# Optimization experiments

Measured on AMD Instinct MI355X. Metric: run time of the kernel, lower is better.

The kernel has to match this reference:

```python
import jax, jax.numpy as jnp
import numpy as np

B, H, W = 8, 160, 160
L = H * W  # 25600, matches nn.LayerNorm(25600)
QDIM = KDIM = MID = OUT = 256
HEADS = 8
HEAD_DIM = MID // HEADS  # 32
LN_EPS = 1e-5


def conv1x1(x, w, b):
    # x: [N,C,H,W], w: [O,C], b: [O] -> [N,O,H,W]
    return jnp.einsum('nchw,oc->nohw', x, w) + b[None, :, None, None]


def setup_inputs() -> dict:
    key = jax.random.key(0)
    ks = jax.random.split(key, 12)
    s = 0.02
    return {
        'query': jax.random.normal(ks[0], (B, QDIM, H, W), jnp.float32),
        'key': jax.random.normal(ks[1], (B, KDIM, H, W), jnp.float32),
        'Wq': jax.random.normal(ks[2], (MID, QDIM), jnp.float32) * s,
        'bq': jnp.zeros((MID,), jnp.float32),
        'Wk': jax.random.normal(ks[3], (MID, KDIM), jnp.float32) * s,
        'bk': jnp.zeros((MID,), jnp.float32),
        'Wv': jax.random.normal(ks[4], (MID, KDIM), jnp.float32) * s,
        'bv': jnp.zeros((MID,), jnp.float32),
        'Wo': jax.random.normal(ks[5], (OUT, MID), jnp.float32) * s,
        'bo': jnp.zeros((OUT,), jnp.float32),
        'gamma': jnp.ones((L,), jnp.float32),
        'beta': jnp.zeros((L,), jnp.float32),
    }


def reference(query, key, Wq, bq, Wk, bk, Wv, bv, Wo, bo, gamma, beta):
    # 1x1-conv projections, flatten spatial dims to L
    q = conv1x1(query, Wq, bq).reshape(B, HEADS, HEAD_DIM, L)
    k = conv1x1(key, Wk, bk).reshape(B, HEADS, HEAD_DIM, L)
    v = conv1x1(key, Wv, bv).reshape(B, HEADS, HEAD_DIM, L)
    # NOTE: faithful to the source, scores contract over L (spatial), giving
    # a [B, heads, head_dim, head_dim] channel-attention matrix.
    scores = jnp.einsum('nhdl,nhel->nhde', q, k) / (KDIM ** 0.5)
    attn = jax.nn.softmax(scores, axis=-1)  # dropout is identity at eval
    out = jnp.einsum('nhde,nhel->nhdl', attn, v).reshape(B, MID, L)
    # LayerNorm over the flattened spatial axis (size 25600)
    mu = jnp.mean(out, axis=-1, keepdims=True)
    var = jnp.var(out, axis=-1, keepdims=True)
    out = (out - mu) * jax.lax.rsqrt(var + LN_EPS) * gamma + beta
    out = out.reshape(B, MID, H, W)
    return conv1x1(out, Wo, bo)
```

## Files before the change

kernel.cpp:

```cpp
#include <hip/hip_runtime.h>
#include <hip/hip_bf16.h>
#include <stdint.h>

#define LROW 25600
#define NCH 256
#define LN_EPS 1e-5f

typedef float f32x4 __attribute__((ext_vector_type(4)));
typedef __bf16 bf16x8 __attribute__((ext_vector_type(8)));
typedef __bf16 bf16x4 __attribute__((ext_vector_type(4)));

__device__ __forceinline__ void gload_lds16(const void* g, void* l) {
  __builtin_amdgcn_global_load_lds(
      (const __attribute__((address_space(1))) void*)(uintptr_t)g,
      (__attribute__((address_space(3))) void*)(uint32_t)(uintptr_t)l,
      16, 0, 0);
}

__device__ __forceinline__ bf16x8 cvt8(f32x4 a, f32x4 b) {
  bf16x8 r;
  r[0] = (__bf16)a[0]; r[1] = (__bf16)a[1]; r[2] = (__bf16)a[2]; r[3] = (__bf16)a[3];
  r[4] = (__bf16)b[0]; r[5] = (__bf16)b[1]; r[6] = (__bf16)b[2]; r[7] = (__bf16)b[3];
  return r;
}

__global__ __launch_bounds__(512, 2) void gram_k(
    const float* __restrict__ qg, const float* __restrict__ kg,
    float* __restrict__ G, float* __restrict__ Gkk,
    float* __restrict__ sq, float* __restrict__ sk) {
  __shared__ __align__(16) float lA[2][8192];
  __shared__ __align__(16) float lB[2][8192];
  const int bid = blockIdx.x;
  const int b = bid >> 5;
  const int s = bid & 31;
  const int mat = (s < 21) ? 0 : 1;
  const int idx = mat ? (s - 21) : s;
  const int parts = mat ? 11 : 21;
  const int c0 = (800 * idx) / parts;
  const int c1 = (800 * (idx + 1)) / parts;
  const int tid = threadIdx.x;
  const int w = tid >> 6, lane = tid & 63;
  const float* Ag = (mat ? kg : qg) + (size_t)b * NCH * LROW;
  const float* Bg = kg + (size_t)b * NCH * LROW;
  float* Gout = (mat ? Gkk : G) + (size_t)b * NCH * NCH;
  float* sums = (mat ? sk : sq) + b * NCH;

  const int rb = w >> 1, chh = w & 1;

  const f32x4 zero = {0.f, 0.f, 0.f, 0.f};
  f32x4 acc[2][4][4];
#pragma unroll
  for (int t = 0; t < 2; ++t)
#pragma unroll
    for (int i = 0; i < 4; ++i)
#pragma unroll
      for (int j = 0; j < 4; ++j) acc[t][i][j] = zero;

  const int cu = (lane & 7) ^ (lane >> 3);

  auto stage = [&](int c, int d) {
#pragma unroll
    for (int i = 0; i < 4; ++i) {
      const int row = (w * 4 + i) * 8 + (lane >> 3);
      gload_lds16(Ag + (size_t)row * LROW + c * 32 + cu * 4, &lA[d][(w * 4 + i) * 256]);
    }
    if (mat == 0) {
#pragma unroll
      for (int i = 0; i < 4; ++i) {
        const int row = (w * 4 + i) * 8 + (lane >> 3);
        gload_lds16(Bg + (size_t)row * LROW + c * 32 + cu * 4, &lB[d][(w * 4 + i) * 256]);
      }
    }
  };

  float rsum = 0.f;
  const int nc = c1 - c0;
  stage(c0, 0);
  for (int cc = 0; cc < nc; ++cc) {
    const int buf = cc & 1;
    const bool pf = (cc + 1 < nc);
    if (pf) stage(c0 + cc + 1, buf ^ 1);
    if (mat == 0) {
      if (pf) asm volatile("s_waitcnt vmcnt(8)" ::: "memory");
      else    asm volatile("s_waitcnt vmcnt(0)" ::: "memory");
    } else {
      if (pf) asm volatile("s_waitcnt vmcnt(4)" ::: "memory");
      else    asm volatile("s_waitcnt vmcnt(0)" ::: "memory");
    }
    __builtin_amdgcn_s_barrier();
    __builtin_amdgcn_sched_barrier(0);

    {
      const int row = tid >> 1;
      const int ub = (tid & 1) * 4;
#pragma unroll
      for (int u = 0; u < 4; ++u) {
        f32x4 v = *(const f32x4*)&lA[buf][row * 32 + (ub + u) * 4];
        rsum += v[0] + v[1] + v[2] + v[3];
      }
    }

    bf16x8 a[4];
#pragma unroll
    for (int i = 0; i < 4; ++i) {
      const int row = rb * 64 + i * 16 + (lane & 15);
      const int u0 = (lane >> 4) * 2;
      const int s0 = u0 ^ (row & 7), s1 = (u0 + 1) ^ (row & 7);
      f32x4 f0 = *(const f32x4*)&lA[buf][row * 32 + s0 * 4];
      f32x4 f1 = *(const f32x4*)&lA[buf][row * 32 + s1 * 4];
      a[i] = cvt8(f0, f1);
    }
    const float(*lBp)[8192] = mat ? lA : lB;
#pragma unroll
    for (int t = 0; t < 2; ++t) {
#pragma unroll
      for (int j = 0; j < 4; ++j) {
        const int row = chh * 128 + t * 64 + j * 16 + (lane & 15);
        const int u0 = (lane >> 4) * 2;
        const int s0 = u0 ^ (row & 7), s1 = (u0 + 1) ^ (row & 7);
        f32x4 f0 = *(const f32x4*)&lBp[buf][row * 32 + s0 * 4];
        f32x4 f1 = *(const f32x4*)&lBp[buf][row * 32 + s1 * 4];
        bf16x8 bfrag = cvt8(f0, f1);
#pragma unroll
        for (int i = 0; i < 4; ++i)
          acc[t][i][j] = __builtin_amdgcn_mfma_f32_16x16x32_bf16(a[i], bfrag, acc[t][i][j], 0, 0, 0);
      }
    }
    asm volatile("s_waitcnt lgkmcnt(0)" ::: "memory");
    __builtin_amdgcn_s_barrier();
    __builtin_amdgcn_sched_barrier(0);
  }

  atomicAdd(&sums[tid >> 1], rsum);
#pragma unroll
  for (int t = 0; t < 2; ++t)
#pragma unroll
    for (int i = 0; i < 4; ++i)
#pragma unroll
      for (int j = 0; j < 4; ++j) {
        const int col = chh * 128 + t * 64 + j * 16 + (lane & 15);
        const int row0 = rb * 64 + i * 16 + (lane >> 4) * 4;
#pragma unroll
        for (int r = 0; r < 4; ++r)
          atomicAdd(&Gout[(row0 + r) * NCH + col], acc[t][i][j][r]);
      }
}

__global__ __launch_bounds__(256) void attn_k(
    const float* __restrict__ G, const float* __restrict__ sq,
    const float* __restrict__ sk,
    const float* __restrict__ Wq, const float* __restrict__ bq,
    const float* __restrict__ Wk, const float* __restrict__ bk,
    const float* __restrict__ Wv, const float* __restrict__ bv,
    float* __restrict__ M, float* __restrict__ cvec) {
  __shared__ float Wql[32][257];
  __shared__ float Wkl[32][257];
  __shared__ float QGl[32][257];
  __shared__ float Sl[32][33];
  __shared__ float Al[32][33];
  __shared__ float ul[32], wl[32];
  const int b = blockIdx.x >> 3, h = blockIdx.x & 7;
  const int t = threadIdx.x;
  const float* Gb = G + (size_t)b * 65536;

  for (int i = 0; i < 32; ++i) {
    int idx = i * 256 + t;
    int d = idx >> 8, c = idx & 255;
    Wql[d][c] = Wq[(h * 32 + d) * 256 + c];
    Wkl[d][c] = Wk[(h * 32 + d) * 256 + c];
  }
  __syncthreads();
  {
    float a[32];
#pragma unroll
    for (int d = 0; d < 32; ++d) a[d] = 0.f;
    for (int c = 0; c < 256; ++c) {
      float g = Gb[c * 256 + t];
#pragma unroll
      for (int d = 0; d < 32; ++d) a[d] += Wql[d][c] * g;
    }
    for (int d = 0; d < 32; ++d) QGl[d][t] = a[d];
  }
  if (t < 32) {
    float u = 0.f, wv = 0.f;
    for (int c = 0; c < 256; ++c) {
      u += Wql[t][c] * sq[b * 256 + c];
      wv += Wkl[t][c] * sk[b * 256 + c];
    }
    ul[t] = u; wl[t] = wv;
  }
  __syncthreads();
  for (int i = 0; i < 4; ++i) {
    int idx = i * 256 + t;
    int d = idx >> 5, e = idx & 31;
    float sv = 0.f;
    for (int c = 0; c < 256; ++c) sv += QGl[d][c] * Wkl[e][c];
    float bqd = bq[h * 32 + d], bke = bk[h * 32 + e];
    Sl[d][e] = (sv + ul[d] * bke + bqd * wl[e] + 25600.f * bqd * bke) * (1.f / 16.f);
  }
  __syncthreads();
  if (t < 32) {
    float m = -1e30f;
    for (int e = 0; e < 32; ++e) m = fmaxf(m, Sl[t][e]);
    float ssum = 0.f;
    for (int e = 0; e < 32; ++e) { float p = __expf(Sl[t][e] - m); Al[t][e] = p; ssum += p; }
    float is = 1.f / ssum;
    for (int e = 0; e < 32; ++e) Al[t][e] *= is;
  }
  __syncthreads();
  {
    float a[32];
#pragma unroll
    for (int d = 0; d < 32; ++d) a[d] = 0.f;
    for (int e = 0; e < 32; ++e) {
      float wv = Wv[(h * 32 + e) * 256 + t];
#pragma unroll
      for (int d = 0; d < 32; ++d) a[d] += Al[d][e] * wv;
    }
    for (int d = 0; d < 32; ++d) M[((size_t)b * 256 + h * 32 + d) * 256 + t] = a[d];
  }
  if (t < 32) {
    float cv = 0.f;
    for (int e = 0; e < 32; ++e) cv += Al[t][e] * bv[h * 32 + e];
    cvec[b * 256 + h * 32 + t] = cv;
  }
}

__global__ __launch_bounds__(256) void stats_k(
    const float* __restrict__ Gkk, const float* __restrict__ M,
    const float* __restrict__ sk, const float* __restrict__ cvec,
    float* __restrict__ mu, float* __restrict__ inv) {
  __shared__ float Ml[32][257];
  __shared__ float Ql[32][257];
  const int b = blockIdx.x >> 3, cb = blockIdx.x & 7;
  const int t = threadIdx.x;
  const float* Gk = Gkk + (size_t)b * 65536;
  for (int i = 0; i < 32; ++i) {
    int idx = i * 256 + t;
    Ml[idx >> 8][idx & 255] = M[((size_t)b * 256 + cb * 32 + (idx >> 8)) * 256 + (idx & 255)];
  }
  __syncthreads();
  {
    float a[32];
#pragma unroll
    for (int c = 0; c < 32; ++c) a[c] = 0.f;
    for (int cc = 0; cc < 256; ++cc) {
      float g = Gk[cc * 256 + t];
#pragma unroll
      for (int c = 0; c < 32; ++c) a[c] += Ml[c][cc] * g;
    }
    for (int c = 0; c < 32; ++c) Ql[c][t] = a[c];
  }
  __syncthreads();
  if (t < 32) {
    float qf = 0.f, msk = 0.f;
    for (int j = 0; j < 256; ++j) {
      qf += Ql[t][j] * Ml[t][j];
      msk += Ml[t][j] * sk[b * 256 + j];
    }
    int c = cb * 32 + t;
    float cv = cvec[b * 256 + c];
    float muv = msk * (1.f / 25600.f) + cv;
    float sum2 = qf + 2.f * cv * msk + 25600.f * cv * cv;
    float var = sum2 * (1.f / 25600.f) - muv * muv;
    mu[b * 256 + c] = muv;
    inv[b * 256 + c] = rsqrtf(var + LN_EPS);
  }
}

__global__ __launch_bounds__(256) void pmat_k(
    const float* __restrict__ M, const float* __restrict__ Wo,
    const float* __restrict__ inv, const float* __restrict__ cvec,
    const float* __restrict__ mu, __bf16* __restrict__ Pb,
    float* __restrict__ t1, float* __restrict__ wsum) {
  __shared__ float Wol[32][257];
  __shared__ float invl[256];
  const int b = blockIdx.x >> 3, ob = blockIdx.x & 7;
  const int t = threadIdx.x;
  invl[t] = inv[b * 256 + t];
  __syncthreads();
  for (int i = 0; i < 32; ++i) {
    int idx = i * 256 + t;
    int o = idx >> 8, c = idx & 255;
    Wol[o][c] = Wo[(ob * 32 + o) * 256 + c] * invl[c];
  }
  __syncthreads();
  {
    float a[32];
#pragma unroll
    for (int o = 0; o < 32; ++o) a[o] = 0.f;
    for (int c = 0; c < 256; ++c) {
      float m = M[((size_t)b * 256 + c) * 256 + t];
#pragma unroll
      for (int o = 0; o < 32; ++o) a[o] += Wol[o][c] * m;
    }
    for (int o = 0; o < 32; ++o)
      Pb[((size_t)b * 256 + ob * 32 + o) * 256 + t] = (__bf16)a[o];
  }
  if (t < 32) {
    float s1 = 0.f, s2 = 0.f;
    for (int c = 0; c < 256; ++c) {
      s1 += Wol[t][c] * (cvec[b * 256 + c] - mu[b * 256 + c]);
      s2 += Wo[(ob * 32 + t) * 256 + c];
    }
    t1[b * 256 + ob * 32 + t] = s1;
    wsum[b * 256 + ob * 32 + t] = s2;
  }
}

__global__ __launch_bounds__(512, 2) void out_k(
    const float* __restrict__ key, const __bf16* __restrict__ Pb,
    const float* __restrict__ t1, const float* __restrict__ wsum,
    const float* __restrict__ bo, const float* __restrict__ gamma,
    const float* __restrict__ beta, float* __restrict__ out) {
  __shared__ __align__(16) __bf16 Bt[256 * 256];
  const int bid = blockIdx.x;
  const int b = bid / 100, tt = bid % 100;
  const int l0 = tt * 256;
  const int tid = threadIdx.x, w = tid >> 6, lane = tid & 63;
  const float* Kb = key + (size_t)b * NCH * LROW;

  for (int i = 0; i < 32; ++i) {
    int idx = i * 512 + tid;
    int l = idx & 255, cq = idx >> 8;
    float x0 = Kb[(size_t)(cq * 4 + 0) * LROW + l0 + l];
    float x1 = Kb[(size_t)(cq * 4 + 1) * LROW + l0 + l];
    float x2 = Kb[(size_t)(cq * 4 + 2) * LROW + l0 + l];
    float x3 = Kb[(size_t)(cq * 4 + 3) * LROW + l0 + l];
    bf16x4 hv;
    hv[0] = (__bf16)x0; hv[1] = (__bf16)x1; hv[2] = (__bf16)x2; hv[3] = (__bf16)x3;
    int unit = cq >> 1;
    int byteoff = l * 512 + (((unit ^ (l & 7))) << 4) + (cq & 1) * 8;
    *(bf16x4*)((char*)Bt + byteoff) = hv;
  }
  __syncthreads();

  const int rb = w >> 1, chh = w & 1;
  const f32x4 zero = {0.f, 0.f, 0.f, 0.f};
  f32x4 acc[2][4][4];
#pragma unroll
  for (int t = 0; t < 2; ++t)
#pragma unroll
    for (int i = 0; i < 4; ++i)
#pragma unroll
      for (int j = 0; j < 4; ++j) acc[t][i][j] = zero;

#pragma unroll
  for (int ks = 0; ks < 8; ++ks) {
    bf16x8 a[4];
#pragma unroll
    for (int i = 0; i < 4; ++i) {
      const int row = rb * 64 + i * 16 + (lane & 15);
      a[i] = *(const bf16x8*)(Pb + ((size_t)b * 256 + row) * 256 + ks * 32 + (lane >> 4) * 8);
    }
#pragma unroll
    for (int t = 0; t < 2; ++t) {
#pragma unroll
      for (int j = 0; j < 4; ++j) {
        const int col = chh * 128 + t * 64 + j * 16 + (lane & 15);
        const int unit = ks * 4 + (lane >> 4);
        const int byteoff = col * 512 + ((unit ^ (col & 7)) << 4);
        bf16x8 bfrag = *(const bf16x8*)((const char*)Bt + byteoff);
#pragma unroll
        for (int i = 0; i < 4; ++i)
          acc[t][i][j] = __builtin_amdgcn_mfma_f32_16x16x32_bf16(a[i], bfrag, acc[t][i][j], 0, 0, 0);
      }
    }
  }

  float t1r[4][4], wsr[4][4], bor[4][4];
#pragma unroll
  for (int i = 0; i < 4; ++i)
#pragma unroll
    for (int r = 0; r < 4; ++r) {
      const int row = rb * 64 + i * 16 + (lane >> 4) * 4 + r;
      t1r[i][r] = t1[b * 256 + row];
      wsr[i][r] = wsum[b * 256 + row];
      bor[i][r] = bo[row];
    }
#pragma unroll
  for (int t = 0; t < 2; ++t)
#pragma unroll
    for (int j = 0; j < 4; ++j) {
      const int col = chh * 128 + t * 64 + j * 16 + (lane & 15);
      const float gm = gamma[l0 + col];
      const float bt = beta[l0 + col];
#pragma unroll
      for (int i = 0; i < 4; ++i) {
        const int row0 = rb * 64 + i * 16 + (lane >> 4) * 4;
#pragma unroll
        for (int r = 0; r < 4; ++r) {
          const int row = row0 + r;
          float v = gm * (acc[t][i][j][r] + t1r[i][r]) + bt * wsr[i][r] + bor[i][r];
          out[((size_t)b * 256 + row) * LROW + l0 + col] = v;
        }
      }
    }
}

extern "C" void kernel_launch(void* const* d_in, const int* in_sizes, int n_in,
                              void* d_out, int out_size, void* d_ws, size_t ws_size,
                              hipStream_t stream) {
  const float* query = (const float*)d_in[0];
  const float* key   = (const float*)d_in[1];
  const float* Wq = (const float*)d_in[2];
  const float* bq = (const float*)d_in[3];
  const float* Wk = (const float*)d_in[4];
  const float* bk = (const float*)d_in[5];
  const float* Wv = (const float*)d_in[6];
  const float* bv = (const float*)d_in[7];
  const float* Wo = (const float*)d_in[8];
  const float* bo = (const float*)d_in[9];
  const float* gamma = (const float*)d_in[10];
  const float* beta  = (const float*)d_in[11];
  float* out = (float*)d_out;

  float* ws = (float*)d_ws;
  float* G    = ws;
  float* Gkk  = G + 524288;
  float* sq   = Gkk + 524288;
  float* sk   = sq + 2048;
  float* M    = sk + 2048;
  float* cvec = M + 524288;
  float* mu   = cvec + 2048;
  float* inv  = mu + 2048;
  float* t1   = inv + 2048;
  float* wsum = t1 + 2048;
  __bf16* Pb  = (__bf16*)(wsum + 2048);

  hipMemsetAsync(d_ws, 0, (size_t)(524288 * 2 + 4096) * sizeof(float), stream);

  gram_k<<<256, 512, 0, stream>>>(query, key, G, Gkk, sq, sk);
  attn_k<<<64, 256, 0, stream>>>(G, sq, sk, Wq, bq, Wk, bk, Wv, bv, M, cvec);
  stats_k<<<64, 256, 0, stream>>>(Gkk, M, sk, cvec, mu, inv);
  pmat_k<<<64, 256, 0, stream>>>(M, Wo, inv, cvec, mu, Pb, t1, wsum);
  out_k<<<800, 512, 0, stream>>>(key, Pb, t1, wsum, bo, gamma, beta, out);
}
```

Before: 571.5 us.

## Cache bf16 key from gram pass, replace atomics with partials, bf16 output GEMM

The gram kernel now converts fp32 tiles to bf16 once, in registers, before writing them to LDS, using register double-buffering in place of direct global-to-LDS loads. The key-only blocks also write a bf16 copy of key to workspace. Partial Gram matrices go to per-split slices and are summed by a new reduce kernel, which removes the atomics and the large memset. The output kernel then reads the half-size bf16 key, cutting its input traffic, in exchange for extra workspace writes and an added reduce launch.

Result: slower. 673.1 us (+17.8%).

```diff
diff --git a/kernel.cpp b/kernel.cpp
--- a/kernel.cpp
+++ b/kernel.cpp
@@ -9,13 +9,7 @@
 typedef float f32x4 __attribute__((ext_vector_type(4)));
 typedef __bf16 bf16x8 __attribute__((ext_vector_type(8)));
 typedef __bf16 bf16x4 __attribute__((ext_vector_type(4)));
-
-__device__ __forceinline__ void gload_lds16(const void* g, void* l) {
-  __builtin_amdgcn_global_load_lds(
-      (const __attribute__((address_space(1))) void*)(uintptr_t)g,
-      (__attribute__((address_space(3))) void*)(uint32_t)(uintptr_t)l,
-      16, 0, 0);
-}
+typedef uint32_t u32x2 __attribute__((ext_vector_type(2)));
 
 __device__ __forceinline__ bf16x8 cvt8(f32x4 a, f32x4 b) {
   bf16x8 r;
@@ -24,126 +18,149 @@
   return r;
 }
 
-__global__ __launch_bounds__(512, 2) void gram_k(
+__device__ __forceinline__ void wg_bar() {
+  asm volatile("s_waitcnt lgkmcnt(0)\n\ts_barrier" ::: "memory");
+}
+
+template <int FULL>
+__global__ __launch_bounds__(1024, 4) void gram_k(
     const float* __restrict__ qg, const float* __restrict__ kg,
-    float* __restrict__ G, float* __restrict__ Gkk,
-    float* __restrict__ sq, float* __restrict__ sk) {
-  __shared__ __align__(16) float lA[2][8192];
-  __shared__ __align__(16) float lB[2][8192];
+    float* __restrict__ Gd, float* __restrict__ Gkkd,
+    float* __restrict__ sq, float* __restrict__ sk,
+    __bf16* __restrict__ kbf) {
+  __shared__ __align__(16) __bf16 lA[256 * 32];
+  __shared__ __align__(16) __bf16 lB[256 * 32];
   const int bid = blockIdx.x;
-  const int b = bid >> 5;
-  const int s = bid & 31;
+  const int b = bid >> 5, s = bid & 31;
   const int mat = (s < 21) ? 0 : 1;
   const int idx = mat ? (s - 21) : s;
   const int parts = mat ? 11 : 21;
-  const int c0 = (800 * idx) / parts;
-  const int c1 = (800 * (idx + 1)) / parts;
+  const int c0 = (800 * idx) / parts, c1 = (800 * (idx + 1)) / parts;
+  const int nc = c1 - c0;
   const int tid = threadIdx.x;
   const int w = tid >> 6, lane = tid & 63;
+  const int wr = w >> 2, wc = w & 3;
+  const int lr = lane & 15, g = lane >> 4;
   const float* Ag = (mat ? kg : qg) + (size_t)b * NCH * LROW;
   const float* Bg = kg + (size_t)b * NCH * LROW;
-  float* Gout = (mat ? Gkk : G) + (size_t)b * NCH * NCH;
-  float* sums = (mat ? sk : sq) + b * NCH;
-
-  const int rb = w >> 1, chh = w & 1;
+
+  const int rowS = tid >> 2, uS = tid & 3;
+  const int uSw = uS ^ ((rowS >> 1) & 3);
+  const size_t gOff = (size_t)rowS * LROW + uS * 8;
+  __bf16* ldsA_dst = lA + rowS * 32 + uSw * 8;
+  __bf16* ldsB_dst = lB + rowS * 32 + uSw * 8;
 
   const f32x4 zero = {0.f, 0.f, 0.f, 0.f};
-  f32x4 acc[2][4][4];
-#pragma unroll
-  for (int t = 0; t < 2; ++t)
+  f32x4 acc[4][4];
+#pragma unroll
+  for (int i = 0; i < 4; ++i)
+#pragma unroll
+    for (int j = 0; j < 4; ++j) acc[i][j] = zero;
+
+  float rsum = 0.f;
+
+  auto LOADG = [&](int c, f32x4* d) {
+    const float* pa = Ag + gOff + (size_t)c * 32;
+    d[0] = *(const f32x4*)pa;
+    d[1] = *(const f32x4*)(pa + 4);
+    if (mat == 0) {
+      const float* pb = Bg + gOff + (size_t)c * 32;
+      d[2] = *(const f32x4*)pb;
+      d[3] = *(const f32x4*)(pb + 4);
+    }
+  };
+
+  auto PROCESS = [&](int c, f32x4* d) {
+#pragma unroll
+    for (int e = 0; e < 4; ++e) rsum += d[0][e] + d[1][e];
+    bf16x8 av = cvt8(d[0], d[1]);
+    *(bf16x8*)ldsA_dst = av;
+    if (mat == 0) {
+      *(bf16x8*)ldsB_dst = cvt8(d[2], d[3]);
+    } else if (FULL) {
+      *(bf16x8*)(kbf + (size_t)(b * NCH + rowS) * LROW + (size_t)c * 32 + uS * 8) = av;
+    }
+    wg_bar();
+    const __bf16* Bp = mat ? lA : lB;
+    bf16x8 af[4];
+#pragma unroll
+    for (int i = 0; i < 4; ++i) {
+      const int row = wr * 64 + i * 16 + lr;
+      const int u = g ^ ((row >> 1) & 3);
+      af[i] = *(const bf16x8*)(lA + row * 32 + u * 8);
+    }
+#pragma unroll
+    for (int j = 0; j < 4; ++j) {
+      const int row = wc * 64 + j * 16 + lr;
+      const int u = g ^ ((row >> 1) & 3);
+      bf16x8 bfj = *(const bf16x8*)(Bp + row * 32 + u * 8);
+#pragma unroll
+      for (int i = 0; i < 4; ++i)
+        acc[i][j] = __builtin_amdgcn_mfma_f32_16x16x32_bf16(af[i], bfj, acc[i][j], 0, 0, 0);
+    }
+    wg_bar();
+  };
+
+  f32x4 bA[4], bB[4];
+  LOADG(c0, bA);
+  int cc = 0;
+  for (; cc + 2 <= nc; cc += 2) {
+    LOADG(c0 + cc + 1, bB);
+    PROCESS(c0 + cc, bA);
+    if (cc + 2 < nc) LOADG(c0 + cc + 2, bA);
+    PROCESS(c0 + cc + 1, bB);
+  }
+  if (cc < nc) PROCESS(c0 + cc, bA);
+
+  atomicAdd((mat ? sk : sq) + b * NCH + rowS, rsum);
+
+  if (FULL) {
+    float* Gout = mat ? (Gkkd + ((size_t)b * 11 + idx) * 65536)
+                      : (Gd + ((size_t)b * 21 + idx) * 65536);
 #pragma unroll
     for (int i = 0; i < 4; ++i)
 #pragma unroll
-      for (int j = 0; j < 4; ++j) acc[t][i][j] = zero;
-
-  const int cu = (lane & 7) ^ (lane >> 3);
-
-  auto stage = [&](int c, int d) {
-#pragma unroll
-    for (int i = 0; i < 4; ++i) {
-      const int row = (w * 4 + i) * 8 + (lane >> 3);
-      gload_lds16(Ag + (size_t)row * LROW + c * 32 + cu * 4, &lA[d][(w * 4 + i) * 256]);
-    }
-    if (mat == 0) {
-#pragma unroll
-      for (int i = 0; i < 4; ++i) {
-        const int row = (w * 4 + i) * 8 + (lane >> 3);
-        gload_lds16(Bg + (size_t)row * LROW + c * 32 + cu * 4, &lB[d][(w * 4 + i) * 256]);
+      for (int j = 0; j < 4; ++j) {
+        const int col = wc * 64 + j * 16 + lr;
+        const int row0 = wr * 64 + i * 16 + g * 4;
+#pragma unroll
+        for (int r = 0; r < 4; ++r)
+          Gout[(size_t)(row0 + r) * NCH + col] = acc[i][j][r];
       }
-    }
-  };
-
-  float rsum = 0.f;
-  const int nc = c1 - c0;
-  stage(c0, 0);
-  for (int cc = 0; cc < nc; ++cc) {
-    const int buf = cc & 1;
-    const bool pf = (cc + 1 < nc);
-    if (pf) stage(c0 + cc + 1, buf ^ 1);
-    if (mat == 0) {
-      if (pf) asm volatile("s_waitcnt vmcnt(8)" ::: "memory");
-      else    asm volatile("s_waitcnt vmcnt(0)" ::: "memory");
-    } else {
-      if (pf) asm volatile("s_waitcnt vmcnt(4)" ::: "memory");
-      else    asm volatile("s_waitcnt vmcnt(0)" ::: "memory");
-    }
-    __builtin_amdgcn_s_barrier();
-    __builtin_amdgcn_sched_barrier(0);
-
-    {
-      const int row = tid >> 1;
-      const int ub = (tid & 1) * 4;
-#pragma unroll
-      for (int u = 0; u < 4; ++u) {
-        f32x4 v = *(const f32x4*)&lA[buf][row * 32 + (ub + u) * 4];
-        rsum += v[0] + v[1] + v[2] + v[3];
+  } else {
+    float* Gout = (mat ? Gkkd : Gd) + (size_t)b * 65536;
+#pragma unroll
+    for (int i = 0; i < 4; ++i)
+#pragma unroll
+      for (int j = 0; j < 4; ++j) {
+        const int col = wc * 64 + j * 16 + lr;
+        const int row0 = wr * 64 + i * 16 + g * 4;
+#pragma unroll
+        for (int r = 0; r < 4; ++r)
+          atomicAdd(&Gout[(size_t)(row0 + r) * NCH + col], acc[i][j][r]);
       }
-    }
-
-    bf16x8 a[4];
-#pragma unroll
-    for (int i = 0; i < 4; ++i) {
-      const int row = rb * 64 + i * 16 + (lane & 15);
-      const int u0 = (lane >> 4) * 2;
-      const int s0 = u0 ^ (row & 7), s1 = (u0 + 1) ^ (row & 7);
-      f32x4 f0 = *(const f32x4*)&lA[buf][row * 32 + s0 * 4];
-      f32x4 f1 = *(const f32x4*)&lA[buf][row * 32 + s1 * 4];
-      a[i] = cvt8(f0, f1);
-    }
-    const float(*lBp)[8192] = mat ? lA : lB;
-#pragma unroll
-    for (int t = 0; t < 2; ++t) {
-#pragma unroll
-      for (int j = 0; j < 4; ++j) {
-        const int row = chh * 128 + t * 64 + j * 16 + (lane & 15);
-        const int u0 = (lane >> 4) * 2;
-        const int s0 = u0 ^ (row & 7), s1 = (u0 + 1) ^ (row & 7);
-        f32x4 f0 = *(const f32x4*)&lBp[buf][row * 32 + s0 * 4];
-        f32x4 f1 = *(const f32x4*)&lBp[buf][row * 32 + s1 * 4];
-        bf16x8 bfrag = cvt8(f0, f1);
-#pragma unroll
-        for (int i = 0; i < 4; ++i)
-          acc[t][i][j] = __builtin_amdgcn_mfma_f32_16x16x32_bf16(a[i], bfrag, acc[t][i][j], 0, 0, 0);
-      }
-    }
-    asm volatile("s_waitcnt lgkmcnt(0)" ::: "memory");
-    __builtin_amdgcn_s_barrier();
-    __builtin_amdgcn_sched_barrier(0);
-  }
-
-  atomicAdd(&sums[tid >> 1], rsum);
-#pragma unroll
-  for (int t = 0; t < 2; ++t)
-#pragma unroll
-    for (int i = 0; i < 4; ++i)
-#pragma unroll
-      for (int j = 0; j < 4; ++j) {
-        const int col = chh * 128 + t * 64 + j * 16 + (lane & 15);
-        const int row0 = rb * 64 + i * 16 + (lane >> 4) * 4;
-#pragma unroll
-        for (int r = 0; r < 4; ++r)
-          atomicAdd(&Gout[(row0 + r) * NCH + col], acc[t][i][j][r]);
-      }
+  }
+}
+
+__global__ __launch_bounds__(256) void reduce_k(
+    const float* __restrict__ Gp, const float* __restrict__ Gkkp,
+    float* __restrict__ Gred, float* __restrict__ Gkkred) {
+  const f32x4 zero = {0.f, 0.f, 0.f, 0.f};
+  if (blockIdx.x < 512) {
+    int f = (blockIdx.x * 256 + threadIdx.x) * 4;
+    int b = f >> 16, r = f & 65535;
+    f32x4 a = zero;
+    for (int si = 0; si < 21; ++si)
+      a += *(const f32x4*)(Gp + ((size_t)b * 21 + si) * 65536 + r);
+    *(f32x4*)(Gred + f) = a;
+  } else {
+    int f = ((blockIdx.x - 512) * 256 + threadIdx.x) * 4;
+    int b = f >> 16, r = f & 65535;
+    f32x4 a = zero;
+    for (int si = 0; si < 11; ++si)
+      a += *(const f32x4*)(Gkkp + ((size_t)b * 11 + si) * 65536 + r);
+    *(f32x4*)(Gkkred + f) = a;
+  }
 }
 
 __global__ __launch_bounds__(256) void attn_k(
@@ -175,9 +192,9 @@
 #pragma unroll
     for (int d = 0; d < 32; ++d) a[d] = 0.f;
     for (int c = 0; c < 256; ++c) {
-      float g = Gb[c * 256 + t];
-#pragma unroll
-      for (int d = 0; d < 32; ++d) a[d] += Wql[d][c] * g;
+      float gv = Gb[c * 256 + t];
+#pragma unroll
+      for (int d = 0; d < 32; ++d) a[d] += Wql[d][c] * gv;
     }
     for (int d = 0; d < 32; ++d) QGl[d][t] = a[d];
   }
@@ -245,9 +262,9 @@
 #pragma unroll
     for (int c = 0; c < 32; ++c) a[c] = 0.f;
     for (int cc = 0; cc < 256; ++cc) {
-      float g = Gk[cc * 256 + t];
-#pragma unroll
-      for (int c = 0; c < 32; ++c) a[c] += Ml[c][cc] * g;
+      float gv = Gk[cc * 256 + t];
+#pragma unroll
+      for (int c = 0; c < 32; ++c) a[c] += Ml[c][cc] * gv;
     }
     for (int c = 0; c < 32; ++c) Ql[c][t] = a[c];
   }
@@ -308,7 +325,95 @@
   }
 }
 
-__global__ __launch_bounds__(512, 2) void out_k(
+__global__ __launch_bounds__(512, 4) void outb_k(
+    const __bf16* __restrict__ kbf, const __bf16* __restrict__ Pb,
+    const float* __restrict__ t1, const float* __restrict__ wsum,
+    const float* __restrict__ bo, const float* __restrict__ gamma,
+    const float* __restrict__ beta, float* __restrict__ out) {
+  __shared__ __align__(16) __bf16 Bt[128 * 256];
+  const int bid = blockIdx.x;
+  const int b = bid / 200, lt = bid % 200, l0 = lt * 128;
+  const int tid = threadIdx.x, w = tid >> 6, lane = tid & 63;
+  const int wr = w >> 1, wc = w & 1;
+  const int lr = lane & 15, g = lane >> 4;
+  const __bf16* Kb = kbf + (size_t)b * NCH * LROW;
+
+#pragma unroll
+  for (int i = 0; i < 8; ++i) {
+    const int cb = i * 32 + w * 4;
+    const __bf16* src = Kb + (size_t)cb * LROW + l0 + lane * 2;
+    uint32_t d0 = *(const uint32_t*)src;
+    uint32_t d1 = *(const uint32_t*)(src + LROW);
+    uint32_t d2 = *(const uint32_t*)(src + 2 * LROW);
+    uint32_t d3 = *(const uint32_t*)(src + 3 * LROW);
+    u32x2 lo, hi;
+    lo[0] = (d0 & 0xffffu) | (d1 << 16);
+    lo[1] = (d2 & 0xffffu) | (d3 << 16);
+    hi[0] = (d0 >> 16) | (d1 & 0xffff0000u);
+    hi[1] = (d2 >> 16) | (d3 & 0xffff0000u);
+    const int unit = i * 4 + (w >> 1), sub = (w & 1) * 8;
+    const int llo = lane * 2, lhi = llo + 1;
+    *(u32x2*)((char*)Bt + llo * 512 + ((unit ^ (llo & 7)) << 4) + sub) = lo;
+    *(u32x2*)((char*)Bt + lhi * 512 + ((unit ^ (lhi & 7)) << 4) + sub) = hi;
+  }
+  __syncthreads();
+
+  const f32x4 zero = {0.f, 0.f, 0.f, 0.f};
+  f32x4 acc[4][4];
+#pragma unroll
+  for (int i = 0; i < 4; ++i)
+#pragma unroll
+    for (int j = 0; j < 4; ++j) acc[i][j] = zero;
+
+  const __bf16* Pbase = Pb + (size_t)b * 65536;
+#pragma unroll
+  for (int ks = 0; ks < 8; ++ks) {
+    bf16x8 af[4];
+#pragma unroll
+    for (int i = 0; i < 4; ++i) {
+      const int row = wr * 64 + i * 16 + lr;
+      af[i] = *(const bf16x8*)(Pbase + (size_t)row * 256 + ks * 32 + g * 8);
+    }
+#pragma unroll
+    for (int j = 0; j < 4; ++j) {
+      const int col = wc * 64 + j * 16 + lr;
+      const int unit = ks * 4 + g;
+      bf16x8 bfj = *(const bf16x8*)((const char*)Bt + col * 512 + ((unit ^ (col & 7)) << 4));
+#pragma unroll
+      for (int i = 0; i < 4; ++i)
+        acc[i][j] = __builtin_amdgcn_mfma_f32_16x16x32_bf16(af[i], bfj, acc[i][j], 0, 0, 0);
+    }
+  }
+
+  float t1r[4][4], wsr[4][4], bor[4][4];
+#pragma unroll
+  for (int i = 0; i < 4; ++i)
+#pragma unroll
+    for (int r = 0; r < 4; ++r) {
+      const int row = wr * 64 + i * 16 + g * 4 + r;
+      t1r[i][r] = t1[b * 256 + row];
+      wsr[i][r] = wsum[b * 256 + row];
+      bor[i][r] = bo[row];
+    }
+#pragma unroll
+  for (int j = 0; j < 4; ++j) {
+    const int colg = l0 + wc * 64 + j * 16 + lr;
+    const float gm = gamma[colg];
+    const float bt = beta[colg];
+#pragma unroll
+    for (int i = 0; i < 4; ++i) {
+      const int row0 = wr * 64 + i * 16 + g * 4;
+#pragma unroll
+      for (int r = 0; r < 4; ++r) {
+        const int row = row0 + r;
+        float v = gm * (acc[i][j][r] + t1r[i][r]) + bt * wsr[i][r] + bor[i][r];
+        out[((size_t)b * 256 + row) * LROW + colg] = v;
+      }
+    }
+  }
+}
+
+__global__ __launch_bounds__(512, 2) void out_f32_k(
     const float* __restrict__ key, const __bf16* __restrict__ Pb,
     const float* __restrict__ t1, const float* __restrict__ wsum,
     const float* __restrict__ bo, const float* __restrict__ gamma,
@@ -427,12 +532,27 @@
   float* t1   = inv + 2048;
   float* wsum = t1 + 2048;
   __bf16* Pb  = (__bf16*)(wsum + 2048);
-
-  hipMemsetAsync(d_ws, 0, (size_t)(524288 * 2 + 4096) * sizeof(float), stream);
-
-  gram_k<<<256, 512, 0, stream>>>(query, key, G, Gkk, sq, sk);
+  __bf16* kbf = (__bf16*)(wsum + 2048 + 262144);
+  float* Gp   = (float*)kbf + 13107200;
+  Gp = ws + 28063744;
+  float* Gkkp = ws + 39073792;
+  const size_t need = (size_t)44840960 * 4;
+  const bool full = ws_size >= need;
+
+  if (full) {
+    hipMemsetAsync(sq, 0, 4096 * sizeof(float), stream);
+    gram_k<1><<<256, 1024, 0, stream>>>(query, key, Gp, Gkkp, sq, sk, kbf);
+    reduce_k<<<1024, 256, 0, stream>>>(Gp, Gkkp, G, Gkk);
+  } else {
+    hipMemsetAsync(d_ws, 0, (size_t)1052672 * sizeof(float), stream);
+    gram_k<0><<<256, 1024, 0, stream>>>(query, key, G, Gkk, sq, sk, nullptr);
+  }
   attn_k<<<64, 256, 0, stream>>>(G, sq, sk, Wq, bq, Wk, bk, Wv, bv, M, cvec);
   stats_k<<<64, 256, 0, stream>>>(Gkk, M, sk, cvec, mu, inv);
   pmat_k<<<64, 256, 0, stream>>>(M, Wo, inv, cvec, mu, Pb, t1, wsum);
-  out_k<<<800, 512, 0, stream>>>(key, Pb, t1, wsum, bo, gamma, beta, out);
-}
+  if (full) {
+    outb_k<<<1600, 512, 0, stream>>>(kbf, Pb, t1, wsum, bo, gamma, beta, out);
+  } else {
+    out_f32_k<<<800, 512, 0, stream>>>(key, Pb, t1, wsum, bo, gamma, beta, out);
+  }
+}
```
